# Kernel tuning notes

Hardware: AMD Instinct MI355X
Metric: run time of the kernel (lower is better)

Reference implementation:

```python
import jax, jax.numpy as jnp
import numpy as np

B, C, H, W = 16, 256, 56, 56
HEADS = 4
C_OUT = 256
K = 3
SQ = 16  # squeeze_rate (C=256 >= 80, so not halved)
BN_EPS = 1e-5


def setup_inputs() -> dict:
    key = jax.random.key(0)
    ks = jax.random.split(key, 9)
    r = C // SQ
    cper = C_OUT // HEADS
    return {
        "x": jax.random.normal(ks[0], (B, C, H, W), dtype=jnp.float32),
        "bn_gamma": 1.0 + 0.1 * jax.random.normal(ks[1], (C,), dtype=jnp.float32),
        "bn_beta": 0.1 * jax.random.normal(ks[2], (C,), dtype=jnp.float32),
        "bn_mean": 0.1 * jax.random.normal(ks[3], (C,), dtype=jnp.float32),
        "bn_var": 0.5 + jax.random.uniform(ks[4], (C,), dtype=jnp.float32),
        "fc1_w": 0.1 * jax.random.normal(ks[5], (HEADS, r, C), dtype=jnp.float32),
        "fc2_w": 0.1 * jax.random.normal(ks[6], (HEADS, C, r), dtype=jnp.float32),
        "fc2_b": jnp.ones((HEADS, C), dtype=jnp.float32),  # init.constant_(bias, 1.0)
        "conv_w": 0.05 * jax.random.normal(ks[7], (HEADS, cper, C, K, K), dtype=jnp.float32),
        "inactive_channels": 192,
    }


def reference(x, bn_gamma, bn_beta, bn_mean, bn_var, fc1_w, fc2_w, fc2_b, conv_w, inactive_channels):
    b, c, h, w = x.shape
    heads = fc1_w.shape[0]
    # BatchNorm (inference, running stats) + ReLU
    inv = jax.lax.rsqrt(bn_var + BN_EPS)
    xn = jax.nn.relu((x - bn_mean[None, :, None, None]) * (bn_gamma * inv)[None, :, None, None]
                     + bn_beta[None, :, None, None])
    # Global average pool -> [b, c]
    x_avg = xn.mean(axis=(2, 3))
    # Per-head SE gate: relu(fc2(relu(fc1(x_avg))))  -> [heads, b, c]
    y1 = jax.nn.relu(jnp.einsum("bc,hrc->hbr", x_avg, fc1_w))
    mask = jax.nn.relu(jnp.einsum("hbr,hcr->hbc", y1, fc2_w) + fc2_b[:, None, :])
    lasso_loss = mask.mean(axis=(1, 2)).sum()  # sum over heads of per-head mean
    # topk smallest -> threshold; zero out mask values <= k-th smallest (detached cmp)
    mask_d = jax.lax.stop_gradient(mask)
    if inactive_channels > 0:
        neg_vals, _ = jax.lax.top_k(-mask_d, inactive_channels)  # k largest of -mask
        thresh = -neg_vals[..., -1:]  # k-th smallest of mask, [heads, b, 1]
        mask_c = jnp.where(mask_d <= thresh, 0.0, mask)
    else:
        mask_c = mask
    # Apply per-head channel mask and stack heads: [b, heads*c, h, w]
    mc = jnp.transpose(mask_c, (1, 0, 2))  # [b, heads, c]
    x_mask = (xn[:, None, :, :, :] * mc[:, :, :, None, None]).reshape(b, heads * c, h, w)
    # Grouped conv (groups=heads), weight [heads*cper, c, K, K]
    wflat = conv_w.reshape(-1, c, K, K)
    out = jax.lax.conv_general_dilated(
        x_mask, wflat, window_strides=(1, 1), padding=[(1, 1), (1, 1)],
        dimension_numbers=("NCHW", "OIHW", "NCHW"), feature_group_count=heads)
    bo, co, ho, wo = out.shape
    out = out.reshape(bo, heads, co // heads, ho, wo).transpose(0, 2, 1, 3, 4).reshape(bo, co, ho, wo)
    return out, lasso_loss
```

## Files before the change

### kernel.cpp

```cpp
#include <hip/hip_runtime.h>
#include <hip/hip_bf16.h>
#include <math.h>

#define B_     16
#define C_     256
#define H_     56
#define W_     56
#define HEADS_ 4
#define CPER_  64
#define R_     16
#define HW_    (H_*W_)
#define BN_EPS_ 1e-5f

typedef short bf16x8 __attribute__((ext_vector_type(8)));
typedef float f32x4  __attribute__((ext_vector_type(4)));

__device__ inline unsigned short f2bf(float f) {
    unsigned int u = __builtin_bit_cast(unsigned int, f);
    u += 0x7fffu + ((u >> 16) & 1u);
    return (unsigned short)(u >> 16);
}

__global__ __launch_bounds__(256) void k_pool(
    const float* __restrict__ x,
    const float* __restrict__ gamma, const float* __restrict__ beta,
    const float* __restrict__ mean,  const float* __restrict__ var,
    float* __restrict__ xavg)
{
    int wv = threadIdx.x >> 6, ln = threadIdx.x & 63;
    int plane = blockIdx.x * 4 + wv;
    int c = plane & (C_ - 1);
    float s = gamma[c] * rsqrtf(var[c] + BN_EPS_);
    float t = fmaf(-mean[c], s, beta[c]);
    const float4* xp = (const float4*)(x + (size_t)plane * HW_);
    float sum = 0.f;
    for (int i = ln; i < HW_ / 4; i += 64) {
        float4 v = xp[i];
        sum += fmaxf(fmaf(v.x, s, t), 0.f) + fmaxf(fmaf(v.y, s, t), 0.f)
             + fmaxf(fmaf(v.z, s, t), 0.f) + fmaxf(fmaf(v.w, s, t), 0.f);
    }
    for (int off = 32; off; off >>= 1) sum += __shfl_down(sum, off, 64);
    if (ln == 0) xavg[plane] = sum * (1.f / HW_);
}

__global__ __launch_bounds__(256) void k_se(
    const float* __restrict__ xavg,
    const float* __restrict__ fc1, const float* __restrict__ fc2,
    const float* __restrict__ fc2b, const int* __restrict__ kptr,
    float* __restrict__ maskc, int* __restrict__ aidx64,
    int* __restrict__ act_cnt, float* __restrict__ lasso)
{
    int hb = blockIdx.x;
    int h = hb / B_, b = hb - h * B_;
    int tid = threadIdx.x;

    __shared__ float sav[C_], sy1[R_], smask[C_], sred[4], sthr;
    __shared__ int scnt, s_ord[C_];

    sav[tid] = xavg[b * C_ + tid];
    if (tid == 0) scnt = 0;
    __syncthreads();

    if (tid < R_) {
        const float* w = fc1 + (size_t)(h * R_ + tid) * C_;
        float acc = 0.f;
        for (int c2 = 0; c2 < C_; ++c2) acc = fmaf(sav[c2], w[c2], acc);
        sy1[tid] = fmaxf(acc, 0.f);
    }
    __syncthreads();

    const float* w2 = fc2 + (size_t)(h * C_ + tid) * R_;
    float acc = fc2b[h * C_ + tid];
    for (int r = 0; r < R_; ++r) acc = fmaf(sy1[r], w2[r], acc);
    float m = fmaxf(acc, 0.f);
    smask[tid] = m;
    __syncthreads();

    float ls = m;
    for (int off = 32; off > 0; off >>= 1) ls += __shfl_down(ls, off, 64);
    int lane = tid & 63, wv = tid >> 6;
    if (lane == 0) sred[wv] = ls;

    int cl = 0, ce = 0;
    for (int j = 0; j < C_; ++j) {
        float vj = smask[j];
        cl += (vj < m);
        ce += (vj == m);
    }
    if (tid == 0) sthr = -1e30f;
    __syncthreads();
    int k = kptr[0];
    if (k > 0 && cl <= k - 1 && (k - 1) < cl + ce) sthr = m;
    __syncthreads();

    float thr = sthr;
    float mc = (m <= thr) ? 0.f : m;
    maskc[hb * C_ + tid] = mc;
    if (mc != 0.f) {
        int p = atomicAdd(&scnt, 1);
        s_ord[p] = tid;
    }
    __syncthreads();
    if (tid < 64) aidx64[hb * 64 + tid] = (tid < scnt) ? s_ord[tid] : 0;
    if (tid == 0) {
        act_cnt[hb] = scnt;
        atomicAdd(lasso, (sred[0] + sred[1] + sred[2] + sred[3]) * (1.f / (B_ * C_)));
    }
}

__global__ __launch_bounds__(256) void k_wgather(
    const float* __restrict__ convw, const float* __restrict__ maskc,
    const int* __restrict__ aidx64, const int* __restrict__ acnt,
    short* __restrict__ Wc)
{
    int hb = blockIdx.x;
    int h = hb >> 4;
    int tid = threadIdx.x;
    int cnt = acnt[hb];
    __shared__ int s_act[64];
    __shared__ float s_mv[64];
    __shared__ short sO[9 * 4096];
    if (tid < 64) {
        int a = aidx64[hb * 64 + tid];
        s_act[tid] = a;
        s_mv[tid]  = (tid < cnt) ? maskc[hb * C_ + a] : 0.f;
    }
    __syncthreads();
    const float* wsrc = convw + (size_t)h * CPER_ * C_ * 9;
    for (int it = 0; it < 16; ++it) {
        int e = it * 256 + tid;
        int cp = e & 63, j = e >> 6;
        const float* wp = wsrc + ((size_t)j * C_ + s_act[cp]) * 9;
        float mv = s_mv[cp];
        int slot = (cp + 8 * (j & 7)) & 63;
        #pragma unroll
        for (int t = 0; t < 9; ++t)
            sO[t * 4096 + j * 64 + slot] = (short)f2bf(wp[t] * mv);
    }
    __syncthreads();
    short* wdst = Wc + (size_t)hb * 9 * 4096;
    for (int it = 0; it < 18; ++it) {
        int e = it * 256 + tid;
        *(bf16x8*)&wdst[e * 8] = *(const bf16x8*)&sO[e * 8];
    }
}

__global__ __launch_bounds__(256) void k_bnc(
    const float* __restrict__ x,
    const float* __restrict__ gamma, const float* __restrict__ beta,
    const float* __restrict__ mean,  const float* __restrict__ var,
    const int* __restrict__ aidx64, short* __restrict__ xc)
{
    int y = blockIdx.x, b = blockIdx.y;
    int tid = threadIdx.x;
    int h = tid >> 6;
    __shared__ __align__(16) unsigned short T[W_ * 256];

    int c = aidx64[(h * B_ + b) * 64 + (tid & 63)];
    float s = gamma[c] * rsqrtf(var[c] + BN_EPS_);
    float t0 = fmaf(-mean[c], s, beta[c]);
    const float* xrow = x + ((size_t)(b * C_ + c)) * HW_ + y * W_;
    #pragma unroll
    for (int f = 0; f < 14; ++f) {
        float4 v = *(const float4*)(xrow + f * 4);
        int px = f * 4;
        T[(px + 0) * 256 + tid] = f2bf(fmaxf(fmaf(v.x, s, t0), 0.f));
        T[(px + 1) * 256 + tid] = f2bf(fmaxf(fmaf(v.y, s, t0), 0.f));
        T[(px + 2) * 256 + tid] = f2bf(fmaxf(fmaf(v.z, s, t0), 0.f));
        T[(px + 3) * 256 + tid] = f2bf(fmaxf(fmaf(v.w, s, t0), 0.f));
    }
    __syncthreads();

    const uint2* Ts = (const uint2*)T;
    uint2* ob = (uint2*)xc;
    #pragma unroll
    for (int it = 0; it < 14; ++it) {
        int e = it * 256 + tid;
        int px = e >> 6, col4 = e & 63;
        int hh = col4 >> 4, cp4 = col4 & 15;
        uint2 v = Ts[px * 64 + col4];
        ob[((size_t)(hh * B_ + b) * HW_ + (size_t)y * W_ + px) * 16 + cp4] = v;
    }
}

__global__ __launch_bounds__(512, 2) void k_conv(
    const short* __restrict__ xc, const short* __restrict__ Wc,
    float* __restrict__ out)
{
    int g = blockIdx.x;
    int vx = g & 7, r = g >> 3;
    int hb = vx * 8 + r / 7;
    int band = r - (r / 7) * 7;
    int h = hb >> 4, b = hb & 15;
    int tid = threadIdx.x, lane = tid & 63, wv = tid >> 6;
    int m = lane & 15, q = lane >> 4;
    int yrow = band * 8 + wv;
    int arot = q * 8 + 8 * (m & 7);

    __shared__ short sW[9 * 4096];

    const short* Wh = Wc + (size_t)hb * 9 * 4096;
    const short* xb = xc + (size_t)hb * HW_ * 64 + q * 8;

    bf16x8 bFb[3][4];
    bf16x8 aFb[2][4];

#define LOADB_(kk) { \
        const int t_ = (kk) >> 1, c0_ = ((kk) & 1) * 32; \
        const int dy_ = t_ / 3 - 1, dx_ = t_ % 3 - 1; \
        int gy_ = yrow + dy_; \
        bool ok_ = (unsigned)gy_ < (unsigned)H_; \
        _Pragma("unroll") \
        for (int xt_ = 0; xt_ < 4; ++xt_) { \
            int gx_ = xt_ * 16 + m + dx_; \
            bf16x8 v_ = {0, 0, 0, 0, 0, 0, 0, 0}; \
            if (ok_ && (unsigned)gx_ < (unsigned)W_) \
                v_ = *(const bf16x8*)(xb + ((size_t)(gy_ * W_ + gx_)) * 64 + c0_); \
            bFb[(kk) % 3][xt_] = v_; \
        } }

#define LOADA_(kk) { \
        const int t_ = (kk) >> 1, c0_ = ((kk) & 1) * 32; \
        const short* sWc_ = sW + t_ * 4096; \
        _Pragma("unroll") \
        for (int jt_ = 0; jt_ < 4; ++jt_) \
            aFb[(kk) % 2][jt_] = *(const bf16x8*)&sWc_[(jt_ * 16 + m) * 64 + ((c0_ + arot) & 63)]; \
        }

    LOADB_(0);
    LOADB_(1);

    #pragma unroll
    for (int it = 0; it < 9; ++it) {
        int e = it * 512 + tid;
        *(bf16x8*)&sW[e * 8] = *(const bf16x8*)(Wh + e * 8);
    }
    __syncthreads();

    f32x4 acc[4][4];
    #pragma unroll
    for (int i = 0; i < 4; ++i)
        #pragma unroll
        for (int j = 0; j < 4; ++j)
            #pragma unroll
            for (int rr = 0; rr < 4; ++rr) acc[i][j][rr] = 0.f;

    LOADA_(0);

    #pragma unroll
    for (int k = 0; k < 18; ++k) {
        if (k + 2 < 18) LOADB_(k + 2);
        if (k + 1 < 18) LOADA_(k + 1);
        #pragma unroll
        for (int jt = 0; jt < 4; ++jt)
            #pragma unroll
            for (int xt = 0; xt < 4; ++xt)
                acc[jt][xt] = __builtin_amdgcn_mfma_f32_16x16x32_bf16(
                    aFb[k % 2][jt], bFb[k % 3][xt], acc[jt][xt], 0, 0, 0);
    }
#undef LOADB_
#undef LOADA_

    #pragma unroll
    for (int xt = 0; xt < 4; ++xt) {
        int xx = xt * 16 + m;
        if (xx < W_) {
            #pragma unroll
            for (int jt = 0; jt < 4; ++jt)
                #pragma unroll
                for (int rr = 0; rr < 4; ++rr) {
                    int j = jt * 16 + q * 4 + rr;
                    int oc = j * HEADS_ + h;
                    out[(((size_t)b * C_ + oc) * H_ + yrow) * W_ + xx] = acc[jt][xt][rr];
                }
        }
    }
}

extern "C" void kernel_launch(void* const* d_in, const int* in_sizes, int n_in,
                              void* d_out, int out_size, void* d_ws, size_t ws_size,
                              hipStream_t stream)
{
    const float* x     = (const float*)d_in[0];
    const float* gamma = (const float*)d_in[1];
    const float* beta  = (const float*)d_in[2];
    const float* mean  = (const float*)d_in[3];
    const float* var   = (const float*)d_in[4];
    const float* fc1   = (const float*)d_in[5];
    const float* fc2   = (const float*)d_in[6];
    const float* fc2b  = (const float*)d_in[7];
    const float* convw = (const float*)d_in[8];
    const int*   kptr  = (const int*)d_in[9];

    float* out   = (float*)d_out;
    float* lasso = out + (size_t)B_ * C_ * HW_;

    char* ws = (char*)d_ws;
    size_t off = 0;
    short* xc    = (short*)(ws + off); off += (size_t)HEADS_ * B_ * HW_ * 64 * 2;
    off = (off + 255) & ~(size_t)255;
    float* xavg  = (float*)(ws + off); off += (size_t)B_ * C_ * 4;
    float* maskc = (float*)(ws + off); off += (size_t)HEADS_ * B_ * C_ * 4;
    int*   aidx64= (int*)  (ws + off); off += (size_t)HEADS_ * B_ * 64 * 4;
    int*   acnt  = (int*)  (ws + off); off += (size_t)HEADS_ * B_ * 4;
    off = (off + 255) & ~(size_t)255;
    short* Wc    = (short*)(ws + off); off += (size_t)HEADS_ * B_ * 9 * CPER_ * 64 * 2;

    hipMemsetAsync(lasso, 0, 4, stream);

    k_pool<<<B_ * C_ / 4, 256, 0, stream>>>(x, gamma, beta, mean, var, xavg);
    k_se<<<HEADS_ * B_, 256, 0, stream>>>(xavg, fc1, fc2, fc2b, kptr,
                                          maskc, aidx64, acnt, lasso);
    k_wgather<<<HEADS_ * B_, 256, 0, stream>>>(convw, maskc, aidx64, acnt, Wc);
    k_bnc<<<dim3(H_, B_), 256, 0, stream>>>(x, gamma, beta, mean, var, aidx64, xc);
    k_conv<<<HEADS_ * B_ * (H_ / 8), 512, 0, stream>>>(xc, Wc, out);
}
```

Before: 195.6 us.

## Fuse SE gate with weight gather and split conv tiles by x-halves

Merges the SE gating kernel with the masked weight gather, which removes one launch and the maskc/act_cnt round trip through global memory. The conv grid is doubled so each block covers half the image width (32 columns), which halves the per-wave accumulators and raises the number of blocks for better occupancy. The B-operand prefetch depth rises from 2 to 3 stages. In exchange, each block now reloads the full weight tile into shared memory, so weight staging traffic doubles, and the fused SE kernel uses a large shared-memory footprint.

```diff
diff --git a/kernel.cpp b/kernel.cpp
--- a/kernel.cpp
+++ b/kernel.cpp
@@ -43,12 +43,13 @@
     if (ln == 0) xavg[plane] = sum * (1.f / HW_);
 }
 
-__global__ __launch_bounds__(256) void k_se(
+__global__ __launch_bounds__(256) void k_se_wg(
     const float* __restrict__ xavg,
     const float* __restrict__ fc1, const float* __restrict__ fc2,
     const float* __restrict__ fc2b, const int* __restrict__ kptr,
-    float* __restrict__ maskc, int* __restrict__ aidx64,
-    int* __restrict__ act_cnt, float* __restrict__ lasso)
+    const float* __restrict__ convw,
+    int* __restrict__ aidx64, float* __restrict__ lasso,
+    short* __restrict__ Wc)
 {
     int hb = blockIdx.x;
     int h = hb / B_, b = hb - h * B_;
@@ -56,6 +57,9 @@
 
     __shared__ float sav[C_], sy1[R_], smask[C_], sred[4], sthr;
     __shared__ int scnt, s_ord[C_];
+    __shared__ int s_act[64];
+    __shared__ float s_mv[64];
+    __shared__ short sO[9 * 4096];
 
     sav[tid] = xavg[b * C_ + tid];
     if (tid == 0) scnt = 0;
@@ -95,37 +99,21 @@
 
     float thr = sthr;
     float mc = (m <= thr) ? 0.f : m;
-    maskc[hb * C_ + tid] = mc;
     if (mc != 0.f) {
         int p = atomicAdd(&scnt, 1);
         s_ord[p] = tid;
     }
     __syncthreads();
-    if (tid < 64) aidx64[hb * 64 + tid] = (tid < scnt) ? s_ord[tid] : 0;
-    if (tid == 0) {
-        act_cnt[hb] = scnt;
+    if (tid < 64) {
+        int a = (tid < scnt) ? s_ord[tid] : 0;
+        aidx64[hb * 64 + tid] = a;
+        s_act[tid] = a;
+        s_mv[tid]  = (tid < scnt) ? smask[a] : 0.f;
+    }
+    if (tid == 0)
         atomicAdd(lasso, (sred[0] + sred[1] + sred[2] + sred[3]) * (1.f / (B_ * C_)));
-    }
-}
-
-__global__ __launch_bounds__(256) void k_wgather(
-    const float* __restrict__ convw, const float* __restrict__ maskc,
-    const int* __restrict__ aidx64, const int* __restrict__ acnt,
-    short* __restrict__ Wc)
-{
-    int hb = blockIdx.x;
-    int h = hb >> 4;
-    int tid = threadIdx.x;
-    int cnt = acnt[hb];
-    __shared__ int s_act[64];
-    __shared__ float s_mv[64];
-    __shared__ short sO[9 * 4096];
-    if (tid < 64) {
-        int a = aidx64[hb * 64 + tid];
-        s_act[tid] = a;
-        s_mv[tid]  = (tid < cnt) ? maskc[hb * C_ + a] : 0.f;
-    }
-    __syncthreads();
+    __syncthreads();
+
     const float* wsrc = convw + (size_t)h * CPER_ * C_ * 9;
     for (int it = 0; it < 16; ++it) {
         int e = it * 256 + tid;
@@ -189,12 +177,14 @@
 {
     int g = blockIdx.x;
     int vx = g & 7, r = g >> 3;
-    int hb = vx * 8 + r / 7;
-    int band = r - (r / 7) * 7;
+    int hb = vx * 8 + r / 14;
+    int sub = r - (r / 14) * 14;
+    int band = sub >> 1, xh = sub & 1;
     int h = hb >> 4, b = hb & 15;
     int tid = threadIdx.x, lane = tid & 63, wv = tid >> 6;
     int m = lane & 15, q = lane >> 4;
     int yrow = band * 8 + wv;
+    int xbase = xh * 32;
     int arot = q * 8 + 8 * (m & 7);
 
     __shared__ short sW[9 * 4096];
@@ -202,7 +192,7 @@
     const short* Wh = Wc + (size_t)hb * 9 * 4096;
     const short* xb = xc + (size_t)hb * HW_ * 64 + q * 8;
 
-    bf16x8 bFb[3][4];
+    bf16x8 bFb[4][2];
     bf16x8 aFb[2][4];
 
 #define LOADB_(kk) { \
@@ -211,12 +201,12 @@
         int gy_ = yrow + dy_; \
         bool ok_ = (unsigned)gy_ < (unsigned)H_; \
         _Pragma("unroll") \
-        for (int xt_ = 0; xt_ < 4; ++xt_) { \
-            int gx_ = xt_ * 16 + m + dx_; \
+        for (int xt_ = 0; xt_ < 2; ++xt_) { \
+            int gx_ = xbase + xt_ * 16 + m + dx_; \
             bf16x8 v_ = {0, 0, 0, 0, 0, 0, 0, 0}; \
             if (ok_ && (unsigned)gx_ < (unsigned)W_) \
                 v_ = *(const bf16x8*)(xb + ((size_t)(gy_ * W_ + gx_)) * 64 + c0_); \
-            bFb[(kk) % 3][xt_] = v_; \
+            bFb[(kk) & 3][xt_] = v_; \
         } }
 
 #define LOADA_(kk) { \
@@ -224,11 +214,12 @@
         const short* sWc_ = sW + t_ * 4096; \
         _Pragma("unroll") \
         for (int jt_ = 0; jt_ < 4; ++jt_) \
-            aFb[(kk) % 2][jt_] = *(const bf16x8*)&sWc_[(jt_ * 16 + m) * 64 + ((c0_ + arot) & 63)]; \
+            aFb[(kk) & 1][jt_] = *(const bf16x8*)&sWc_[(jt_ * 16 + m) * 64 + ((c0_ + arot) & 63)]; \
         }
 
     LOADB_(0);
     LOADB_(1);
+    LOADB_(2);
 
     #pragma unroll
     for (int it = 0; it < 9; ++it) {
@@ -237,11 +228,11 @@
     }
     __syncthreads();
 
-    f32x4 acc[4][4];
+    f32x4 acc[4][2];
     #pragma unroll
     for (int i = 0; i < 4; ++i)
         #pragma unroll
-        for (int j = 0; j < 4; ++j)
+        for (int j = 0; j < 2; ++j)
             #pragma unroll
             for (int rr = 0; rr < 4; ++rr) acc[i][j][rr] = 0.f;
 
@@ -249,21 +240,21 @@
 
     #pragma unroll
     for (int k = 0; k < 18; ++k) {
-        if (k + 2 < 18) LOADB_(k + 2);
+        if (k + 3 < 18) LOADB_(k + 3);
         if (k + 1 < 18) LOADA_(k + 1);
         #pragma unroll
         for (int jt = 0; jt < 4; ++jt)
             #pragma unroll
-            for (int xt = 0; xt < 4; ++xt)
+            for (int xt = 0; xt < 2; ++xt)
                 acc[jt][xt] = __builtin_amdgcn_mfma_f32_16x16x32_bf16(
-                    aFb[k % 2][jt], bFb[k % 3][xt], acc[jt][xt], 0, 0, 0);
+                    aFb[k & 1][jt], bFb[k & 3][xt], acc[jt][xt], 0, 0, 0);
     }
 #undef LOADB_
 #undef LOADA_
 
     #pragma unroll
-    for (int xt = 0; xt < 4; ++xt) {
-        int xx = xt * 16 + m;
+    for (int xt = 0; xt < 2; ++xt) {
+        int xx = xbase + xt * 16 + m;
         if (xx < W_) {
             #pragma unroll
             for (int jt = 0; jt < 4; ++jt)
@@ -300,18 +291,15 @@
     short* xc    = (short*)(ws + off); off += (size_t)HEADS_ * B_ * HW_ * 64 * 2;
     off = (off + 255) & ~(size_t)255;
     float* xavg  = (float*)(ws + off); off += (size_t)B_ * C_ * 4;
-    float* maskc = (float*)(ws + off); off += (size_t)HEADS_ * B_ * C_ * 4;
     int*   aidx64= (int*)  (ws + off); off += (size_t)HEADS_ * B_ * 64 * 4;
-    int*   acnt  = (int*)  (ws + off); off += (size_t)HEADS_ * B_ * 4;
     off = (off + 255) & ~(size_t)255;
     short* Wc    = (short*)(ws + off); off += (size_t)HEADS_ * B_ * 9 * CPER_ * 64 * 2;
 
     hipMemsetAsync(lasso, 0, 4, stream);
 
     k_pool<<<B_ * C_ / 4, 256, 0, stream>>>(x, gamma, beta, mean, var, xavg);
-    k_se<<<HEADS_ * B_, 256, 0, stream>>>(xavg, fc1, fc2, fc2b, kptr,
-                                          maskc, aidx64, acnt, lasso);
-    k_wgather<<<HEADS_ * B_, 256, 0, stream>>>(convw, maskc, aidx64, acnt, Wc);
+    k_se_wg<<<HEADS_ * B_, 256, 0, stream>>>(xavg, fc1, fc2, fc2b, kptr, convw,
+                                             aidx64, lasso, Wc);
     k_bnc<<<dim3(H_, B_), 256, 0, stream>>>(x, gamma, beta, mean, var, aidx64, xc);
-    k_conv<<<HEADS_ * B_ * (H_ / 8), 512, 0, stream>>>(xc, Wc, out);
-}
+    k_conv<<<HEADS_ * B_ * 14, 512, 0, stream>>>(xc, Wc, out);
+}
```

After: 193.6 us. About the same (-1.0%).
